# Optimization experiments

Measured on AMD Instinct MI355X. Metric: run time of the kernel, lower is better.

The kernel has to match this reference:

```python
import jax, jax.numpy as jnp
import numpy as np

N, F, H, C = 50000, 128, 4, 32   # nodes, in_channels, heads, hidden_channels
E, R, DE = 800000, 8, 64         # edges, num_relations, edge_dim


def setup_inputs() -> dict:
    key = jax.random.key(0)
    ks = jax.random.split(key, 10)
    x = jax.random.normal(ks[0], (N, F), dtype=jnp.float32)
    edge_index = jax.random.randint(ks[1], (2, E), 0, N, dtype=jnp.int64)
    edge_type = jax.random.randint(ks[2], (E,), 0, R, dtype=jnp.int64)
    s_in = 1.0 / np.sqrt(F)
    s_e = 1.0 / np.sqrt(DE)
    edge_emb = jax.random.normal(ks[3], (R, DE), dtype=jnp.float32)
    Wq = jax.random.normal(ks[4], (F, H * C), dtype=jnp.float32) * s_in
    Wk = jax.random.normal(ks[5], (F, H * C), dtype=jnp.float32) * s_in
    Wv = jax.random.normal(ks[6], (F, H * C), dtype=jnp.float32) * s_in
    We = jax.random.normal(ks[7], (DE, H * C), dtype=jnp.float32) * s_e
    Wskip = jax.random.normal(ks[8], (F, H * C), dtype=jnp.float32) * s_in
    return {"x": x, "edge_index": edge_index, "edge_type": edge_type,
            "edge_emb": edge_emb, "Wq": Wq, "Wk": Wk, "Wv": Wv,
            "We": We, "Wskip": Wskip}


def reference(x, edge_index, edge_type, edge_emb, Wq, Wk, Wv, We, Wskip):
    # TransformerConv (PyG) with edge embeddings, concat heads, root skip, no bias.
    src, dst = edge_index[0], edge_index[1]
    q = (x @ Wq).reshape(N, H, C)
    k = (x @ Wk).reshape(N, H, C)
    v = (x @ Wv).reshape(N, H, C)
    e = (edge_emb[edge_type] @ We).reshape(E, H, C)      # per-edge relation emb
    kj = k[src] + e                                       # [E,H,C]
    logits = (q[dst] * kj).sum(-1) / jnp.sqrt(jnp.float32(C))  # [E,H]
    # segment softmax over incoming edges of each target node
    m = jax.ops.segment_max(logits, dst, num_segments=N)  # [N,H]
    m = jnp.where(jnp.isfinite(m), m, jnp.float32(0.0))
    ex = jnp.exp(logits - m[dst])
    denom = jax.ops.segment_sum(ex, dst, num_segments=N)  # [N,H]
    alpha = ex / (denom[dst] + 1e-16)                     # [E,H]
    msg = (v[src] + e) * alpha[:, :, None]                # [E,H,C]
    out = jax.ops.segment_sum(msg, dst, num_segments=N).reshape(N, H * C)
    return out + x @ Wskip
```

## Files before the change

### kernel.cpp

```cpp
#include <hip/hip_runtime.h>
#include <hip/hip_bf16.h>

#define NN 50000
#define FF 128
#define NH 4
#define CH 32
#define HC 128
#define NE 800000
#define NR 8
#define DEDIM 64
#define NBLK 196
#define HBLK 3125
#define QBLK 250
#define MTILES 3125

typedef __hip_bfloat16 bf16;
typedef __attribute__((ext_vector_type(8))) short short8;
typedef __attribute__((ext_vector_type(4))) float f32x4;

__device__ __forceinline__ float bflo(unsigned u) { return __uint_as_float(u << 16); }
__device__ __forceinline__ float bfhi(unsigned u) { return __uint_as_float(u & 0xFFFF0000u); }

__device__ __forceinline__ unsigned short f2bf(float f) {
  unsigned u = __float_as_uint(f);
  unsigned r = (u + 0x7FFFu + ((u >> 16) & 1u)) >> 16;
  return (unsigned short)r;
}
__device__ __forceinline__ unsigned pack2bf(float lo, float hi) {
  return (unsigned)f2bf(lo) | ((unsigned)f2bf(hi) << 16);
}

template <int ISBF>
__device__ __forceinline__ float ldf(const void* p, size_t i) {
  if (ISBF) return __bfloat162float(((const bf16*)p)[i]);
  return ((const float*)p)[i];
}

__device__ __forceinline__ int idx_at(const void* p, long long i, int is64) {
  if (is64) { long long v = ((const long long*)p)[i]; return (int)v; }
  return ((const int*)p)[i];
}

#define WT_STRIDE 136

template <int ISBF>
__device__ __forceinline__ void stage_w(const void* __restrict__ W,
                                        unsigned short* __restrict__ wt) {
  for (int i = threadIdx.x; i < FF * HC; i += 256) {
    int k = i >> 7, n = i & 127;
    wt[n * WT_STRIDE + k] = ISBF ? ((const unsigned short*)W)[i]
                                 : f2bf(((const float*)W)[i]);
  }
}

__device__ __forceinline__ void hoist_b(const unsigned short* __restrict__ wt,
                                        int wv, int quad, int lr,
                                        short8 bf[2][4]) {
#pragma unroll
  for (int t = 0; t < 2; ++t) {
    int ncol = wv * 32 + t * 16 + lr;
#pragma unroll
    for (int kb = 0; kb < 4; ++kb)
      bf[t][kb] = *(const short8*)&wt[ncol * WT_STRIDE + kb * 32 + quad * 8];
  }
}

template <int ISBF, int GRP>
__device__ __forceinline__ void qkvs_body(const void* __restrict__ x,
    const void* __restrict__ W0, const void* __restrict__ W1, int mc,
    unsigned short* __restrict__ qb, unsigned* __restrict__ kvb,
    void* __restrict__ out, unsigned short* wt) {
  const int lane = threadIdx.x & 63;
  const int wv   = threadIdx.x >> 6;
  const int quad = lane >> 4;
  const int lr   = lane & 15;
  short8 bf0[2][4], bf1[2][4];
  stage_w<ISBF>(W0, wt);
  __syncthreads();
  hoist_b(wt, wv, quad, lr, bf0);
  __syncthreads();
  stage_w<ISBF>(W1, wt);
  __syncthreads();
  hoist_b(wt, wv, quad, lr, bf1);
  const unsigned short* xu = (const unsigned short*)x;
  const float* xf = (const float*)x;
  for (int mt = mc; mt < MTILES; mt += QBLK) {
    int m0 = mt * 16;
    short8 af[4];
#pragma unroll
    for (int kb = 0; kb < 4; ++kb) {
      size_t off = (size_t)(m0 + lr) * FF + kb * 32 + quad * 8;
      if (ISBF) {
        af[kb] = *(const short8*)(xu + off);
      } else {
        float4 fa = *(const float4*)(xf + off);
        float4 fb = *(const float4*)(xf + off + 4);
        short8 a;
        a[0] = (short)f2bf(fa.x); a[1] = (short)f2bf(fa.y);
        a[2] = (short)f2bf(fa.z); a[3] = (short)f2bf(fa.w);
        a[4] = (short)f2bf(fb.x); a[5] = (short)f2bf(fb.y);
        a[6] = (short)f2bf(fb.z); a[7] = (short)f2bf(fb.w);
        af[kb] = a;
      }
    }
    f32x4 a00 = {0.f, 0.f, 0.f, 0.f}, a01 = {0.f, 0.f, 0.f, 0.f};
    f32x4 a10 = {0.f, 0.f, 0.f, 0.f}, a11 = {0.f, 0.f, 0.f, 0.f};
#pragma unroll
    for (int kb = 0; kb < 4; ++kb) {
      a00 = __builtin_amdgcn_mfma_f32_16x16x32_bf16(af[kb], bf0[0][kb], a00, 0, 0, 0);
      a01 = __builtin_amdgcn_mfma_f32_16x16x32_bf16(af[kb], bf0[1][kb], a01, 0, 0, 0);
      a10 = __builtin_amdgcn_mfma_f32_16x16x32_bf16(af[kb], bf1[0][kb], a10, 0, 0, 0);
      a11 = __builtin_amdgcn_mfma_f32_16x16x32_bf16(af[kb], bf1[1][kb], a11, 0, 0, 0);
    }
#pragma unroll
    for (int t = 0; t < 2; ++t) {
      const f32x4 v0 = t ? a01 : a00;
      const f32x4 v1 = t ? a11 : a10;
      int col = wv * 32 + t * 16 + lr;
#pragma unroll
      for (int r = 0; r < 4; ++r) {
        size_t oi = (size_t)(m0 + quad * 4 + r) * HC + col;
        if (GRP == 0) {
          qb[oi] = f2bf(v0[r]);
          if (ISBF) ((unsigned short*)out)[oi] = f2bf(v1[r]);
          else      ((float*)out)[oi] = v1[r];
        } else {
          kvb[oi] = pack2bf(v0[r], v1[r]);
        }
      }
    }
  }
}

__global__ __launch_bounds__(256) void k_fusedA(const unsigned* __restrict__ xw,
    const int* __restrict__ eidx32, const void* __restrict__ etype,
    const void* __restrict__ emb, const void* __restrict__ We,
    const void* __restrict__ Wq, const void* __restrict__ Ws,
    const void* __restrict__ Wk, const void* __restrict__ Wv,
    int* __restrict__ flag, int* __restrict__ hist, float* __restrict__ ee,
    unsigned* __restrict__ drk, int* __restrict__ setp,
    unsigned short* __restrict__ qb, unsigned* __restrict__ kvb,
    void* __restrict__ out) {
  __shared__ unsigned short wt[HC * WT_STRIDE];
  if (blockIdx.x < 2 * QBLK) {
    unsigned ex = (xw[threadIdx.x & 63] >> 7) & 0xFFu;
    unsigned long long bb = __ballot(ex < 90u || ex > 140u);
    int isbf = (bb == 0ULL);
    if (blockIdx.x < QBLK) {
      if (isbf) qkvs_body<1, 0>(xw, Wq, Ws, blockIdx.x, qb, kvb, out, wt);
      else      qkvs_body<0, 0>(xw, Wq, Ws, blockIdx.x, qb, kvb, out, wt);
    } else {
      int mc = blockIdx.x - QBLK;
      if (isbf) qkvs_body<1, 1>(xw, Wk, Wv, mc, qb, kvb, out, wt);
      else      qkvs_body<0, 1>(xw, Wk, Wv, mc, qb, kvb, out, wt);
    }
    return;
  }
  if (blockIdx.x < 2 * QBLK + HBLK) {
    unsigned long long b = __ballot(eidx32[2 * (threadIdx.x & 63) + 1] != 0);
    int is64 = (b == 0ULL);
    int e = (blockIdx.x - 2 * QBLK) * 256 + threadIdx.x;
    int src = idx_at(eidx32, e, is64);
    int dst = idx_at(eidx32, (long long)NE + e, is64);
    int et  = idx_at(etype, e, is64);
    src = min(max(src, 0), NN - 1);
    dst = min(max(dst, 0), NN - 1);
    et  = min(max(et, 0), NR - 1);
    int rank = atomicAdd(&hist[dst], 1);
    drk[e]  = ((unsigned)dst << 16) | ((unsigned)rank & 0xFFFFu);
    setp[e] = (src << 3) | et;
    return;
  }
  float* es = (float*)wt;
  __shared__ int nzIdx, badBf;
  if (threadIdx.x == 0) { nzIdx = 0; badBf = 0; }
  __syncthreads();
  if (threadIdx.x < 128) {
    if (eidx32[2 * threadIdx.x + 1] != 0) atomicAdd(&nzIdx, 1);
    unsigned e = (xw[threadIdx.x] >> 7) & 0xFFu;
    if (e < 90u || e > 140u) atomicAdd(&badBf, 1);
  }
  __syncthreads();
  const int isbf = (badBf == 0);
  if (threadIdx.x == 0) { flag[0] = (nzIdx == 0); flag[1] = isbf; }
  for (int i = threadIdx.x; i < NR * DEDIM; i += 256)
    es[i] = isbf ? ldf<1>(emb, i) : ldf<0>(emb, i);
  __syncthreads();
  for (int o = threadIdx.x; o < NR * HC; o += 256) {
    int r = o >> 7, j = o & 127;
    float acc = 0.f;
    if (isbf) { for (int d = 0; d < DEDIM; ++d) acc += es[r * DEDIM + d] * ldf<1>(We, d * HC + j); }
    else      { for (int d = 0; d < DEDIM; ++d) acc += es[r * DEDIM + d] * ldf<0>(We, d * HC + j); }
    ee[o] = acc;
  }
}

__global__ __launch_bounds__(256) void k_scan1(const int* __restrict__ hist,
                                               int* __restrict__ bsum) {
  __shared__ int red[4];
  int i = blockIdx.x * 256 + threadIdx.x;
  int v = (i < NN) ? hist[i] : 0;
#pragma unroll
  for (int m = 1; m < 64; m <<= 1) v += __shfl_xor(v, m);
  if ((threadIdx.x & 63) == 0) red[threadIdx.x >> 6] = v;
  __syncthreads();
  if (threadIdx.x == 0) bsum[blockIdx.x] = red[0] + red[1] + red[2] + red[3];
}

__global__ __launch_bounds__(256) void k_scan13(const int* __restrict__ hist,
    const int* __restrict__ bsum, int* __restrict__ rowptr) {
  __shared__ int s[256];
  int t = threadIdx.x;
  int bv = (t < NBLK) ? bsum[t] : 0;
  s[t] = bv;
  __syncthreads();
  for (int off = 1; off < 256; off <<= 1) {
    int u = (t >= off) ? s[t - off] : 0;
    __syncthreads();
    s[t] += u;
    __syncthreads();
  }
  int bexc = (blockIdx.x == 0) ? 0 : s[blockIdx.x - 1];
  __syncthreads();
  int i = blockIdx.x * 256 + t;
  int v = (i < NN) ? hist[i] : 0;
  s[t] = v;
  __syncthreads();
  for (int off = 1; off < 256; off <<= 1) {
    int u = (t >= off) ? s[t - off] : 0;
    __syncthreads();
    s[t] += u;
    __syncthreads();
  }
  int excl = bexc + s[t] - v;
  if (i < NN) rowptr[i] = excl;
  if (i == 0) rowptr[NN] = NE;
}

__global__ __launch_bounds__(256) void k_scatter(const unsigned* __restrict__ drk,
    const int* __restrict__ setp, const int* __restrict__ rowptr,
    int* __restrict__ srcet) {
  int e = blockIdx.x * 256 + threadIdx.x;
  unsigned d = drk[e];
  int pos = rowptr[d >> 16] + (int)(d & 0xFFFFu);
  pos = min(max(pos, 0), NE - 1);
  srcet[pos] = setp[e];
}

__global__ __launch_bounds__(256) void k_gather(const int* __restrict__ rowptr,
    const int* __restrict__ srcet, const unsigned short* __restrict__ qb,
    const unsigned* __restrict__ kvb, const float* __restrict__ ee,
    const int* __restrict__ flag, void* __restrict__ out) {
  int n = blockIdx.x * 4 + (threadIdx.x >> 6);
  int l = threadIdx.x & 63;
  int t = l >> 5;
  int w = l & 31;
  int j0 = ((w >> 3) << 5) + ((w & 7) << 2);
  int beg = __builtin_amdgcn_readfirstlane(rowptr[n]);
  int end = __builtin_amdgcn_readfirstlane(rowptr[n + 1]);
  uint2 qw = *(const uint2*)(qb + (size_t)n * HC + j0);
  float q0 = bflo(qw.x), q1 = bfhi(qw.x), q2 = bflo(qw.y), q3 = bfhi(qw.y);
  const float sc = 0.17677669529663687f;
  float dn = 0.f, a0 = 0.f, a1 = 0.f, a2 = 0.f, a3 = 0.f;
  int p = beg;
  for (; p + 8 <= end; p += 8) {
    int se[4]; uint4 kv[4]; float4 ev[4];
#pragma unroll
    for (int u = 0; u < 4; ++u) se[u] = srcet[p + 2 * u + t];
#pragma unroll
    for (int u = 0; u < 4; ++u)
      kv[u] = *(const uint4*)(kvb + (size_t)(se[u] >> 3) * HC + j0);
#pragma unroll
    for (int u = 0; u < 4; ++u)
      ev[u] = *(const float4*)(ee + ((se[u] & 7) << 7) + j0);
#pragma unroll
    for (int u = 0; u < 4; ++u) {
      float pp = q0 * (bflo(kv[u].x) + ev[u].x) + q1 * (bflo(kv[u].y) + ev[u].y)
               + q2 * (bflo(kv[u].z) + ev[u].z) + q3 * (bflo(kv[u].w) + ev[u].w);
      pp += __shfl_xor(pp, 1);
      pp += __shfl_xor(pp, 2);
      pp += __shfl_xor(pp, 4);
      float xx = __expf(pp * sc);
      dn += xx;
      a0 += (bfhi(kv[u].x) + ev[u].x) * xx;
      a1 += (bfhi(kv[u].y) + ev[u].y) * xx;
      a2 += (bfhi(kv[u].z) + ev[u].z) * xx;
      a3 += (bfhi(kv[u].w) + ev[u].w) * xx;
    }
  }
  if (p < end) {
    int se[4]; bool ok[4]; uint4 kv[4]; float4 ev[4];
#pragma unroll
    for (int u = 0; u < 4; ++u) {
      int pe = p + 2 * u + t;
      ok[u] = pe < end;
      se[u] = srcet[ok[u] ? pe : beg];
    }
#pragma unroll
    for (int u = 0; u < 4; ++u)
      kv[u] = *(const uint4*)(kvb + (size_t)(se[u] >> 3) * HC + j0);
#pragma unroll
    for (int u = 0; u < 4; ++u)
      ev[u] = *(const float4*)(ee + ((se[u] & 7) << 7) + j0);
#pragma unroll
    for (int u = 0; u < 4; ++u) {
      float pp = q0 * (bflo(kv[u].x) + ev[u].x) + q1 * (bflo(kv[u].y) + ev[u].y)
               + q2 * (bflo(kv[u].z) + ev[u].z) + q3 * (bflo(kv[u].w) + ev[u].w);
      pp += __shfl_xor(pp, 1);
      pp += __shfl_xor(pp, 2);
      pp += __shfl_xor(pp, 4);
      float xx = ok[u] ? __expf(pp * sc) : 0.f;
      dn += xx;
      a0 += (bfhi(kv[u].x) + ev[u].x) * xx;
      a1 += (bfhi(kv[u].y) + ev[u].y) * xx;
      a2 += (bfhi(kv[u].z) + ev[u].z) * xx;
      a3 += (bfhi(kv[u].w) + ev[u].w) * xx;
    }
  }
  dn += __shfl_xor(dn, 32);
  a0 += __shfl_xor(a0, 32);
  a1 += __shfl_xor(a1, 32);
  a2 += __shfl_xor(a2, 32);
  a3 += __shfl_xor(a3, 32);
  if (t == 0) {
    float inv = 1.f / (dn + 1e-16f);
    size_t oi = (size_t)n * HC + j0;
    if (flag[1]) {
      uint2 sk = *(const uint2*)((const unsigned short*)out + oi);
      uint2 o;
      o.x = pack2bf(a0 * inv + bflo(sk.x), a1 * inv + bfhi(sk.x));
      o.y = pack2bf(a2 * inv + bflo(sk.y), a3 * inv + bfhi(sk.y));
      *(uint2*)((unsigned short*)out + oi) = o;
    } else {
      float4 sk = *(const float4*)((const float*)out + oi);
      float4 o = make_float4(a0 * inv + sk.x, a1 * inv + sk.y,
                             a2 * inv + sk.z, a3 * inv + sk.w);
      *(float4*)((float*)out + oi) = o;
    }
  }
}

extern "C" void kernel_launch(void* const* d_in, const int* in_sizes, int n_in,
                              void* d_out, int out_size, void* d_ws, size_t ws_size,
                              hipStream_t stream) {
  const void* x     = d_in[0];
  const void* eidx  = d_in[1];
  const void* etype = d_in[2];
  const void* emb   = d_in[3];
  const void* Wq    = d_in[4];
  const void* Wk    = d_in[5];
  const void* Wv    = d_in[6];
  const void* We    = d_in[7];
  const void* Ws    = d_in[8];

  float* base   = (float*)d_ws;
  int*   flag   = (int*)base;
  float* ee     = base + 16;
  int*   rowptr = (int*)(base + 1040);
  int*   bsum   = (int*)(base + 51044);
  int*   srcet  = (int*)(base + 101568);
  int*   hist   = srcet;
  unsigned* drk = (unsigned*)(base + 901568);
  int*   setp   = (int*)(base + 1701568);
  unsigned short* qb  = (unsigned short*)(base + 2501568);
  unsigned*       kvb = (unsigned*)(base + 5701568);

  hipMemsetAsync(hist, 0, NN * sizeof(int), stream);
  k_fusedA<<<2 * QBLK + HBLK + 1, 256, 0, stream>>>((const unsigned*)x,
                                                    (const int*)eidx, etype, emb, We,
                                                    Wq, Ws, Wk, Wv, flag, hist, ee,
                                                    drk, setp, qb, kvb, d_out);
  k_scan1  <<<NBLK, 256, 0, stream>>>(hist, bsum);
  k_scan13 <<<NBLK, 256, 0, stream>>>(hist, bsum, rowptr);
  k_scatter<<<HBLK, 256, 0, stream>>>(drk, setp, rowptr, srcet);
  k_gather <<<NN / 4, 256, 0, stream>>>(rowptr, srcet, qb, kvb, ee, flag, d_out);
}
```

Baseline: 253.3 us.

## Split projection GEMM into dedicated kernel computing all four weights per tile

Moves the Q/K/V/skip projection out of the fused prep kernel into its own kernel, where each block stages all four weight matrices in LDS and computes them from a single read of each x tile. The x tile for the next iteration is prefetched while the current one is multiplied. Outputs are staged through LDS so that global stores become coalesced 16-byte writes. The cost is an extra kernel launch, one block per CU because of the large LDS and register footprint, and the loss of overlap between the projection and the edge-preprocessing blocks.

```diff
diff --git a/kernel.cpp b/kernel.cpp
--- a/kernel.cpp
+++ b/kernel.cpp
@@ -41,125 +41,17 @@
   return ((const int*)p)[i];
 }
 
-#define WT_STRIDE 136
-
-template <int ISBF>
-__device__ __forceinline__ void stage_w(const void* __restrict__ W,
-                                        unsigned short* __restrict__ wt) {
-  for (int i = threadIdx.x; i < FF * HC; i += 256) {
-    int k = i >> 7, n = i & 127;
-    wt[n * WT_STRIDE + k] = ISBF ? ((const unsigned short*)W)[i]
-                                 : f2bf(((const float*)W)[i]);
-  }
-}
-
-__device__ __forceinline__ void hoist_b(const unsigned short* __restrict__ wt,
-                                        int wv, int quad, int lr,
-                                        short8 bf[2][4]) {
-#pragma unroll
-  for (int t = 0; t < 2; ++t) {
-    int ncol = wv * 32 + t * 16 + lr;
-#pragma unroll
-    for (int kb = 0; kb < 4; ++kb)
-      bf[t][kb] = *(const short8*)&wt[ncol * WT_STRIDE + kb * 32 + quad * 8];
-  }
-}
-
-template <int ISBF, int GRP>
-__device__ __forceinline__ void qkvs_body(const void* __restrict__ x,
-    const void* __restrict__ W0, const void* __restrict__ W1, int mc,
-    unsigned short* __restrict__ qb, unsigned* __restrict__ kvb,
-    void* __restrict__ out, unsigned short* wt) {
-  const int lane = threadIdx.x & 63;
-  const int wv   = threadIdx.x >> 6;
-  const int quad = lane >> 4;
-  const int lr   = lane & 15;
-  short8 bf0[2][4], bf1[2][4];
-  stage_w<ISBF>(W0, wt);
-  __syncthreads();
-  hoist_b(wt, wv, quad, lr, bf0);
-  __syncthreads();
-  stage_w<ISBF>(W1, wt);
-  __syncthreads();
-  hoist_b(wt, wv, quad, lr, bf1);
-  const unsigned short* xu = (const unsigned short*)x;
-  const float* xf = (const float*)x;
-  for (int mt = mc; mt < MTILES; mt += QBLK) {
-    int m0 = mt * 16;
-    short8 af[4];
-#pragma unroll
-    for (int kb = 0; kb < 4; ++kb) {
-      size_t off = (size_t)(m0 + lr) * FF + kb * 32 + quad * 8;
-      if (ISBF) {
-        af[kb] = *(const short8*)(xu + off);
-      } else {
-        float4 fa = *(const float4*)(xf + off);
-        float4 fb = *(const float4*)(xf + off + 4);
-        short8 a;
-        a[0] = (short)f2bf(fa.x); a[1] = (short)f2bf(fa.y);
-        a[2] = (short)f2bf(fa.z); a[3] = (short)f2bf(fa.w);
-        a[4] = (short)f2bf(fb.x); a[5] = (short)f2bf(fb.y);
-        a[6] = (short)f2bf(fb.z); a[7] = (short)f2bf(fb.w);
-        af[kb] = a;
-      }
-    }
-    f32x4 a00 = {0.f, 0.f, 0.f, 0.f}, a01 = {0.f, 0.f, 0.f, 0.f};
-    f32x4 a10 = {0.f, 0.f, 0.f, 0.f}, a11 = {0.f, 0.f, 0.f, 0.f};
-#pragma unroll
-    for (int kb = 0; kb < 4; ++kb) {
-      a00 = __builtin_amdgcn_mfma_f32_16x16x32_bf16(af[kb], bf0[0][kb], a00, 0, 0, 0);
-      a01 = __builtin_amdgcn_mfma_f32_16x16x32_bf16(af[kb], bf0[1][kb], a01, 0, 0, 0);
-      a10 = __builtin_amdgcn_mfma_f32_16x16x32_bf16(af[kb], bf1[0][kb], a10, 0, 0, 0);
-      a11 = __builtin_amdgcn_mfma_f32_16x16x32_bf16(af[kb], bf1[1][kb], a11, 0, 0, 0);
-    }
-#pragma unroll
-    for (int t = 0; t < 2; ++t) {
-      const f32x4 v0 = t ? a01 : a00;
-      const f32x4 v1 = t ? a11 : a10;
-      int col = wv * 32 + t * 16 + lr;
-#pragma unroll
-      for (int r = 0; r < 4; ++r) {
-        size_t oi = (size_t)(m0 + quad * 4 + r) * HC + col;
-        if (GRP == 0) {
-          qb[oi] = f2bf(v0[r]);
-          if (ISBF) ((unsigned short*)out)[oi] = f2bf(v1[r]);
-          else      ((float*)out)[oi] = v1[r];
-        } else {
-          kvb[oi] = pack2bf(v0[r], v1[r]);
-        }
-      }
-    }
-  }
-}
-
-__global__ __launch_bounds__(256) void k_fusedA(const unsigned* __restrict__ xw,
+__global__ __launch_bounds__(256) void k_prep(const unsigned* __restrict__ xw,
     const int* __restrict__ eidx32, const void* __restrict__ etype,
     const void* __restrict__ emb, const void* __restrict__ We,
-    const void* __restrict__ Wq, const void* __restrict__ Ws,
-    const void* __restrict__ Wk, const void* __restrict__ Wv,
     int* __restrict__ flag, int* __restrict__ hist, float* __restrict__ ee,
-    unsigned* __restrict__ drk, int* __restrict__ setp,
-    unsigned short* __restrict__ qb, unsigned* __restrict__ kvb,
-    void* __restrict__ out) {
-  __shared__ unsigned short wt[HC * WT_STRIDE];
-  if (blockIdx.x < 2 * QBLK) {
-    unsigned ex = (xw[threadIdx.x & 63] >> 7) & 0xFFu;
-    unsigned long long bb = __ballot(ex < 90u || ex > 140u);
-    int isbf = (bb == 0ULL);
-    if (blockIdx.x < QBLK) {
-      if (isbf) qkvs_body<1, 0>(xw, Wq, Ws, blockIdx.x, qb, kvb, out, wt);
-      else      qkvs_body<0, 0>(xw, Wq, Ws, blockIdx.x, qb, kvb, out, wt);
-    } else {
-      int mc = blockIdx.x - QBLK;
-      if (isbf) qkvs_body<1, 1>(xw, Wk, Wv, mc, qb, kvb, out, wt);
-      else      qkvs_body<0, 1>(xw, Wk, Wv, mc, qb, kvb, out, wt);
-    }
-    return;
-  }
-  if (blockIdx.x < 2 * QBLK + HBLK) {
+    unsigned* __restrict__ drk, int* __restrict__ setp) {
+  __shared__ float es[NR * DEDIM];
+  __shared__ int nzIdx, badBf;
+  if (blockIdx.x < HBLK) {
     unsigned long long b = __ballot(eidx32[2 * (threadIdx.x & 63) + 1] != 0);
     int is64 = (b == 0ULL);
-    int e = (blockIdx.x - 2 * QBLK) * 256 + threadIdx.x;
+    int e = blockIdx.x * 256 + threadIdx.x;
     int src = idx_at(eidx32, e, is64);
     int dst = idx_at(eidx32, (long long)NE + e, is64);
     int et  = idx_at(etype, e, is64);
@@ -171,8 +63,6 @@
     setp[e] = (src << 3) | et;
     return;
   }
-  float* es = (float*)wt;
-  __shared__ int nzIdx, badBf;
   if (threadIdx.x == 0) { nzIdx = 0; badBf = 0; }
   __syncthreads();
   if (threadIdx.x < 128) {
@@ -193,6 +83,189 @@
     else      { for (int d = 0; d < DEDIM; ++d) acc += es[r * DEDIM + d] * ldf<0>(We, d * HC + j); }
     ee[o] = acc;
   }
+}
+
+template <int ISBF>
+__device__ __forceinline__ void stage_nat(const void* __restrict__ W,
+                                          unsigned short* __restrict__ w) {
+  if (ISBF) {
+    const uint4* s = (const uint4*)W;
+    uint4* d = (uint4*)w;
+    for (int i = threadIdx.x; i < FF * HC / 8; i += 256) d[i] = s[i];
+  } else {
+    const float4* s = (const float4*)W;
+    short8* d = (short8*)w;
+    for (int i = threadIdx.x; i < FF * HC / 8; i += 256) {
+      float4 a = s[2 * i], b = s[2 * i + 1];
+      short8 o;
+      o[0] = (short)f2bf(a.x); o[1] = (short)f2bf(a.y);
+      o[2] = (short)f2bf(a.z); o[3] = (short)f2bf(a.w);
+      o[4] = (short)f2bf(b.x); o[5] = (short)f2bf(b.y);
+      o[6] = (short)f2bf(b.z); o[7] = (short)f2bf(b.w);
+      d[i] = o;
+    }
+  }
+}
+
+__device__ __forceinline__ void hoist_nat(const unsigned short* __restrict__ w,
+                                          int wv, int quad, int lr,
+                                          short8 bf[2][4]) {
+#pragma unroll
+  for (int t = 0; t < 2; ++t) {
+    int ncol = wv * 32 + t * 16 + lr;
+#pragma unroll
+    for (int kb = 0; kb < 4; ++kb) {
+      short8 v;
+#pragma unroll
+      for (int j = 0; j < 8; ++j)
+        v[j] = (short)w[(kb * 32 + quad * 8 + j) * HC + ncol];
+      bf[t][kb] = v;
+    }
+  }
+}
+
+template <int ISBF>
+__device__ __forceinline__ void qkvs4_body(const void* __restrict__ x,
+    const void* __restrict__ Wq, const void* __restrict__ Ws,
+    const void* __restrict__ Wk, const void* __restrict__ Wv,
+    unsigned short* __restrict__ qb, unsigned* __restrict__ kvb,
+    void* __restrict__ out, unsigned short* __restrict__ wt4,
+    unsigned char* __restrict__ est) {
+  const int tid  = threadIdx.x;
+  const int lane = tid & 63;
+  const int wv   = tid >> 6;
+  const int quad = lane >> 4;
+  const int lr   = lane & 15;
+  stage_nat<ISBF>(Wq, wt4 + 0 * FF * HC);
+  stage_nat<ISBF>(Ws, wt4 + 1 * FF * HC);
+  stage_nat<ISBF>(Wk, wt4 + 2 * FF * HC);
+  stage_nat<ISBF>(Wv, wt4 + 3 * FF * HC);
+  __syncthreads();
+  short8 bf[4][2][4];
+#pragma unroll
+  for (int m = 0; m < 4; ++m)
+    hoist_nat(wt4 + m * FF * HC, wv, quad, lr, bf[m]);
+  unsigned short* qs  = (unsigned short*)est;
+  unsigned short* sbs = (unsigned short*)(est + 4096);
+  float*          sfs = (float*)(est + 4096);
+  unsigned*       kvs = (unsigned*)est;
+  const unsigned short* xu = (const unsigned short*)x;
+  const float* xf = (const float*)x;
+  const int mc = blockIdx.x;
+  short8 lda[4];
+  float4 raw[8];
+  {
+    size_t off = (size_t)(mc * 16 + lr) * FF + quad * 8;
+    if (ISBF) {
+#pragma unroll
+      for (int kb = 0; kb < 4; ++kb) lda[kb] = *(const short8*)(xu + off + kb * 32);
+    } else {
+#pragma unroll
+      for (int kb = 0; kb < 4; ++kb) {
+        raw[2 * kb]     = *(const float4*)(xf + off + kb * 32);
+        raw[2 * kb + 1] = *(const float4*)(xf + off + kb * 32 + 4);
+      }
+    }
+  }
+  for (int mt = mc; mt < MTILES; mt += QBLK) {
+    int m0 = mt * 16;
+    short8 cur[4];
+    if (ISBF) {
+#pragma unroll
+      for (int kb = 0; kb < 4; ++kb) cur[kb] = lda[kb];
+    } else {
+#pragma unroll
+      for (int kb = 0; kb < 4; ++kb) {
+        float4 a = raw[2 * kb], b = raw[2 * kb + 1];
+        short8 o;
+        o[0] = (short)f2bf(a.x); o[1] = (short)f2bf(a.y);
+        o[2] = (short)f2bf(a.z); o[3] = (short)f2bf(a.w);
+        o[4] = (short)f2bf(b.x); o[5] = (short)f2bf(b.y);
+        o[6] = (short)f2bf(b.z); o[7] = (short)f2bf(b.w);
+        cur[kb] = o;
+      }
+    }
+    int mtn = mt + QBLK;
+    if (mtn < MTILES) {
+      size_t off = (size_t)(mtn * 16 + lr) * FF + quad * 8;
+      if (ISBF) {
+#pragma unroll
+        for (int kb = 0; kb < 4; ++kb) lda[kb] = *(const short8*)(xu + off + kb * 32);
+      } else {
+#pragma unroll
+        for (int kb = 0; kb < 4; ++kb) {
+          raw[2 * kb]     = *(const float4*)(xf + off + kb * 32);
+          raw[2 * kb + 1] = *(const float4*)(xf + off + kb * 32 + 4);
+        }
+      }
+    }
+    f32x4 acc[4][2];
+#pragma unroll
+    for (int m = 0; m < 4; ++m)
+#pragma unroll
+      for (int t = 0; t < 2; ++t) acc[m][t] = {0.f, 0.f, 0.f, 0.f};
+#pragma unroll
+    for (int kb = 0; kb < 4; ++kb)
+#pragma unroll
+      for (int m = 0; m < 4; ++m) {
+        acc[m][0] = __builtin_amdgcn_mfma_f32_16x16x32_bf16(cur[kb], bf[m][0][kb], acc[m][0], 0, 0, 0);
+        acc[m][1] = __builtin_amdgcn_mfma_f32_16x16x32_bf16(cur[kb], bf[m][1][kb], acc[m][1], 0, 0, 0);
+      }
+#pragma unroll
+    for (int t = 0; t < 2; ++t)
+#pragma unroll
+      for (int r = 0; r < 4; ++r) {
+        int li = (quad * 4 + r) * HC + wv * 32 + t * 16 + lr;
+        qs[li] = f2bf(acc[0][t][r]);
+        if (ISBF) sbs[li] = f2bf(acc[1][t][r]);
+        else      sfs[li] = acc[1][t][r];
+      }
+    __syncthreads();
+    {
+      int row = tid >> 4, seg = tid & 15;
+      *(uint4*)(qb + (size_t)(m0 + row) * HC + seg * 8) = ((const uint4*)qs)[tid];
+      if (ISBF) {
+        *(uint4*)((unsigned short*)out + (size_t)(m0 + row) * HC + seg * 8) =
+            ((const uint4*)sbs)[tid];
+      } else {
+#pragma unroll
+        for (int s = 0; s < 2; ++s) {
+          int idx = s * 256 + tid, rw = idx >> 5, sg = idx & 31;
+          *(uint4*)((float*)out + (size_t)(m0 + rw) * HC + sg * 4) =
+              ((const uint4*)sfs)[idx];
+        }
+      }
+    }
+    __syncthreads();
+#pragma unroll
+    for (int t = 0; t < 2; ++t)
+#pragma unroll
+      for (int r = 0; r < 4; ++r) {
+        int li = (quad * 4 + r) * HC + wv * 32 + t * 16 + lr;
+        kvs[li] = pack2bf(acc[2][t][r], acc[3][t][r]);
+      }
+    __syncthreads();
+#pragma unroll
+    for (int s = 0; s < 2; ++s) {
+      int idx = s * 256 + tid, rw = idx >> 5, sg = idx & 31;
+      *(uint4*)(kvb + (size_t)(m0 + rw) * HC + sg * 4) = ((const uint4*)kvs)[idx];
+    }
+    __syncthreads();
+  }
+}
+
+__global__ __launch_bounds__(256, 1) void k_qkvs(const unsigned* __restrict__ xw,
+    const void* __restrict__ Wq, const void* __restrict__ Ws,
+    const void* __restrict__ Wk, const void* __restrict__ Wv,
+    unsigned short* __restrict__ qb, unsigned* __restrict__ kvb,
+    void* __restrict__ out) {
+  __shared__ __align__(16) unsigned short wt4[4 * FF * HC];
+  __shared__ __align__(16) unsigned char  est[12288];
+  unsigned ex = (xw[threadIdx.x & 63] >> 7) & 0xFFu;
+  unsigned long long bb = __ballot(ex < 90u || ex > 140u);
+  int isbf = (bb == 0ULL);
+  if (isbf) qkvs4_body<1>(xw, Wq, Ws, Wk, Wv, qb, kvb, out, wt4, est);
+  else      qkvs4_body<0>(xw, Wq, Ws, Wk, Wv, qb, kvb, out, wt4, est);
 }
 
 __global__ __launch_bounds__(256) void k_scan1(const int* __restrict__ hist,
@@ -366,10 +439,11 @@
   unsigned*       kvb = (unsigned*)(base + 5701568);
 
   hipMemsetAsync(hist, 0, NN * sizeof(int), stream);
-  k_fusedA<<<2 * QBLK + HBLK + 1, 256, 0, stream>>>((const unsigned*)x,
-                                                    (const int*)eidx, etype, emb, We,
-                                                    Wq, Ws, Wk, Wv, flag, hist, ee,
-                                                    drk, setp, qb, kvb, d_out);
+  k_prep   <<<HBLK + 1, 256, 0, stream>>>((const unsigned*)x, (const int*)eidx,
+                                          etype, emb, We, flag, hist, ee,
+                                          drk, setp);
+  k_qkvs   <<<QBLK, 256, 0, stream>>>((const unsigned*)x, Wq, Ws, Wk, Wv,
+                                      qb, kvb, d_out);
   k_scan1  <<<NBLK, 256, 0, stream>>>(hist, bsum);
   k_scan13 <<<NBLK, 256, 0, stream>>>(hist, bsum, rowptr);
   k_scatter<<<HBLK, 256, 0, stream>>>(drk, setp, rowptr, srcet);
```

Measured after the change: 265.1 us. 1.05x slower.
